# Optimization experiments

Hardware: AMD Instinct MI355X
Metric: run time of the kernel (lower is better)

Reference implementation:

```python
import jax, jax.numpy as jnp
import numpy as np

# --- config constants (from init_kwargs) ---
ALPHA = 0.05; SIGMA = 0.2; THETA = 0.3; A = 0.02; B_PAR = 0.1; RHO = 0.5
MULT = 2.0          # config.x_range_final[1]
GAMMA = 0.5         # power-utility exponent: u(x,r)=r*x^g/g, ux=r*x^(g-1)
N_STEPS = 100; T_FINAL = 1.0; DT = T_FINAL / N_STEPS
HID = 64; BATCH = 16384
PEN_SCALE = 100.0; LOWER = 1e-6


def _mlp(W1, b1, W2, b2, W3, b3, s):
    # tiny FeedForwardSubNet: 3 -> HID -> HID -> 1, tanh activations
    h = jnp.tanh(s @ W1 + b1)
    h = jnp.tanh(h @ W2 + b2)
    return h @ W3 + b3


def _penalise(v):
    # penalise_range(v, lower): quadratic hinge below `lower`
    return PEN_SCALE * jnp.square(jnp.maximum(LOWER - v, 0.0))


def setup_inputs() -> dict:
    key = jax.random.key(0)
    ks = jax.random.split(key, 16)
    dw = jax.random.normal(ks[0], (BATCH, 1, N_STEPS), dtype=jnp.float32) * float(np.sqrt(DT))
    X0 = jnp.ones((1,), jnp.float32)
    R0 = jnp.ones((1,), jnp.float32)
    def w(k, shape, fan):
        return jax.random.normal(k, shape, jnp.float32) / np.float32(np.sqrt(fan))
    inp = {"dw": dw, "X0": X0, "R0": R0,
           "pW1": w(ks[1], (3, HID), 3), "pb1": jnp.zeros((HID,), jnp.float32),
           "pW2": w(ks[2], (HID, HID), HID), "pb2": jnp.zeros((HID,), jnp.float32),
           "pW3": w(ks[3], (HID, 1), HID), "pb3": jnp.zeros((1,), jnp.float32),
           "qW1": w(ks[4], (3, HID), 3), "qb1": jnp.zeros((HID,), jnp.float32),
           "qW2": w(ks[5], (HID, HID), HID), "qb2": jnp.zeros((HID,), jnp.float32),
           "qW3": w(ks[6], (HID, 1), HID), "qb3": jnp.zeros((1,), jnp.float32)}
    return inp


def reference(dw, X0, R0, pW1, pb1, pW2, pb2, pW3, pb3, qW1, qb1, qW2, qb2, qW3, qb3):
    Bn = dw.shape[0]
    ones = jnp.ones((Bn, 1), dw.dtype)
    times = jnp.arange(N_STEPS + 1, dtype=dw.dtype) * DT   # [N+1]
    x0 = ones * X0
    R0v = ones * R0
    b_eff = float(np.sign(RHO)) * B_PAR

    # p_0 and dp_0 = d p_0 / d x (per-sample, rowwise independent net)
    def p_of_x(xx):
        st = jnp.concatenate([MULT * times[0] * ones, xx, R0v], 1)
        return _mlp(pW1, pb1, pW2, pb2, pW3, pb3, st)
    p0, p_vjp = jax.vjp(p_of_x, x0)
    (dp0,) = p_vjp(jnp.ones_like(p0))
    pi0 = _mlp(qW1, qb1, qW2, qb2, qW3, qb3,
               jnp.concatenate([MULT * times[0] * ones, x0, R0v], 1))

    dw_t = jnp.transpose(dw, (2, 0, 1))          # [N, B, 1]
    upd = jnp.arange(N_STEPS) < (N_STEPS - 1)    # pi not updated at last step

    def step(carry, inp):
        x, min_x, W, pi = carry
        dwi, t_next, u = inp
        x = x + x * ALPHA * DT + pi * SIGMA * THETA * DT + pi * SIGMA * dwi
        min_x = jnp.minimum(x, min_x)
        W = W + dwi
        Rv = R0v * jnp.exp((A - 0.5 * b_eff ** 2) * t_next + b_eff * W)
        p = p0 * jnp.exp(-(ALPHA + 0.5 * THETA ** 2) * t_next - THETA * W)
        st = jnp.concatenate([MULT * t_next * jnp.ones_like(x), x, Rv], 1)
        pi_new = _mlp(qW1, qb1, qW2, qb2, qW3, qb3, st)
        pi = jnp.where(u, pi_new, pi)
        return (x, min_x, W, pi), (x, Rv, pi, -p)

    (xf, min_x, Wf, pif), (xs, Rs, pis, dMs) = jax.lax.scan(
        step, (x0, x0, jnp.zeros_like(x0), pi0), (dw_t, times[1:], upd))

    # stacked process data, matching tf.concat-over-axis-0 ordering: [(N+1)*B, 1]
    x_all  = jnp.concatenate([x0[None], xs], 0).reshape(-1, 1)
    r_all  = jnp.concatenate([R0v[None], Rs], 0).reshape(-1, 1)
    pi_all = jnp.concatenate([pi0[None], pis], 0).reshape(-1, 1)
    dM_all = jnp.concatenate([(-p0)[None], dMs], 0).reshape(-1, 1)
    dM2_all = jnp.tile(-dp0, (N_STEPS + 1, 1))
    proc = jnp.concatenate([x_all, r_all, pi_all, dM_all, dM2_all], 1)  # [(N+1)*B, 5]

    # losses (non_concave = False branch)
    p_fin = -dMs[-1]
    R_fin = Rs[-1]
    xc = jnp.maximum(xf, LOWER)
    ux = R_fin * xc ** (GAMMA - 1.0)
    u_val = R_fin * xc ** GAMMA / GAMMA
    pen = _penalise(min_x)
    loss_p = jnp.mean(jnp.square(p_fin + ux) + pen)
    loss_pi = loss_p + jnp.mean(-u_val + pen)

    return jnp.concatenate([proc.reshape(-1), jnp.stack([loss_p, loss_pi])])
```

## Files before the change

kernel.cpp:

```cpp
#include <hip/hip_runtime.h>
#include <hip/hip_bf16.h>
#include <math.h>

#define NSTEP 100
#define BATCH 16384
#define MB 16
#define NBLK (BATCH/MB)
#define NT 256

#define C_ALPHA 0.05f
#define C_SIGMA 0.2f
#define C_THETA 0.3f
#define C_DT    0.01f
#define C_LOWER 1e-6f
#define C_PEN   100.0f
#define LOG2E   1.4426950408889634f
#define TSCALE  (2.0f * LOG2E)
#define CRT ( 0.015f * C_DT * LOG2E)
#define CRW ( 0.1f * LOG2E)
#define CPT (-0.095f * C_DT * LOG2E)
#define CPW (-0.3f * LOG2E)

#define TSC   64.0f
#define TOFF  512.0f
#define TMAX  1023.999f
#define AXD   (1.0f + C_ALPHA * C_DT)
#define SIGTHDT (C_SIGMA * C_THETA * C_DT)

#define WG_BARRIER() asm volatile("s_waitcnt lgkmcnt(0)\n\ts_barrier" ::: "memory")

typedef __attribute__((ext_vector_type(8))) short bf16x8;
typedef __attribute__((ext_vector_type(4))) float f32x4;
typedef __attribute__((ext_vector_type(4), aligned(4))) float f32x4a;

__device__ __forceinline__ float tanh_pre(float zs) {
    float e = __builtin_amdgcn_exp2f(zs);
    return 1.0f - 2.0f * __builtin_amdgcn_rcpf(e + 1.0f);
}
__device__ __forceinline__ unsigned f2bf_u(float f) {
    unsigned u = __float_as_uint(f);
    return (u + 0x7FFFu + ((u >> 16) & 1u)) >> 16;
}
__device__ __forceinline__ unsigned pack_bf16(float a, float b) {
    union { __hip_bfloat162 h; unsigned u; } cv;
    cv.h = __float22bfloat162_rn(make_float2(a, b));
    return cv.u;
}
__device__ __forceinline__ float dpp_row_sum16(float v) {
    int t;
    t = __builtin_amdgcn_update_dpp(0, __float_as_int(v), 0x128, 0xF, 0xF, true);
    v += __int_as_float(t);
    t = __builtin_amdgcn_update_dpp(0, __float_as_int(v), 0x124, 0xF, 0xF, true);
    v += __int_as_float(t);
    t = __builtin_amdgcn_update_dpp(0, __float_as_int(v), 0x122, 0xF, 0xF, true);
    v += __int_as_float(t);
    t = __builtin_amdgcn_update_dpp(0, __float_as_int(v), 0x121, 0xF, 0xF, true);
    v += __int_as_float(t);
    return v;
}

__global__ __launch_bounds__(NT, 4) void fused_kernel(
        const float* __restrict__ dw, const float* __restrict__ X0,
        const float* __restrict__ R0,
        const float* __restrict__ pW1, const float* __restrict__ pb1,
        const float* __restrict__ pW2, const float* __restrict__ pb2,
        const float* __restrict__ pW3, const float* __restrict__ pb3,
        const float* __restrict__ qW1, const float* __restrict__ qb1,
        const float* __restrict__ qW2, const float* __restrict__ qb2,
        const float* __restrict__ qW3, const float* __restrict__ qb3,
        float* __restrict__ ws, float* __restrict__ out) {
    __shared__ __align__(16) unsigned short sW2T[64 * 72];
    __shared__ __align__(16) float sdw[MB * NSTEP];
    __shared__ __align__(16) float2 sTab[1024];
    __shared__ __align__(16) uint2 sA2[2][2][64][2];
    __shared__ __align__(16) float sPb[2][2][16][2];

    const int tid = threadIdx.x;
    const int lane = tid & 63;
    const int wv = tid >> 6;
    const int ks_own = wv >> 1;
    const int half = wv & 1;
    const int b0 = blockIdx.x * MB;
    const int l15 = lane & 15, quad = lane >> 4;

    {
        const float4* g = (const float4*)(dw + (size_t)b0 * NSTEP);
        float4* s = (float4*)sdw;
        for (int u = tid; u < MB * NSTEP / 4; u += NT) s[u] = g[u];
    }
    for (int u4 = tid; u4 < 1024; u4 += NT) {
        float4 w = ((const float4*)qW2)[u4];
        int base = u4 * 4;
        int k = base >> 6, n = base & 63;
        sW2T[(n + 0) * 72 + k] = (unsigned short)f2bf_u(w.x * TSC);
        sW2T[(n + 1) * 72 + k] = (unsigned short)f2bf_u(w.y * TSC);
        sW2T[(n + 2) * 72 + k] = (unsigned short)f2bf_u(w.z * TSC);
        sW2T[(n + 3) * 72 + k] = (unsigned short)f2bf_u(w.w * TSC);
    }
    for (int u = tid; u < 1024; u += NT) {
        float z0 = (float)u * (1.0f / TSC) - 8.0f;
        float t0 = tanh_pre(TSCALE * z0);
        float t1 = tanh_pre(TSCALE * (z0 + 1.0f / TSC));
        sTab[u] = make_float2(t0, t1 - t0);
    }
    __syncthreads();

    auto tab = [&](float u) -> float {
        float uc = __builtin_amdgcn_fmed3f(u, 0.0f, TMAX);
        int idx = (int)uc;
        float f = uc - (float)idx;
        float2 e = sTab[idx];
        return fmaf(f, e.y, e.x);
    };

    bf16x8 Bw0, Bw1;
    {
        const unsigned short* rp = &sW2T[(wv * 16 + l15) * 72 + quad * 8];
        Bw0 = *(const bf16x8*)rp;
        Bw1 = *(const bf16x8*)(rp + 32);
    }
    float tco[4], w1xs[4], w1rs[4], b1s[4];
    {
        const int kb = ks_own * 32 + quad * 8 + half * 4;
        #pragma unroll
        for (int j = 0; j < 4; j++) {
            tco[j]  = qW1[kb + j] * (2.0f * C_DT * TSC);
            w1xs[j] = qW1[64 + kb + j] * TSC;
            w1rs[j] = qW1[128 + kb + j] * TSC;
            b1s[j]  = qb1[kb + j] * TSC + TOFF;
        }
    }
    f32x4 b2w;
    float w3w[4];
    #pragma unroll
    for (int r = 0; r < 4; r++) {
        b2w[r] = qb2[wv * 16 + quad * 4 + r] * TSC + TOFF;
        w3w[r] = qW3[wv * 16 + quad * 4 + r];
    }
    const float b3 = qb3[0];
    const float X0v = X0[0], R0s = R0[0];

    uint2*       wA0 = &sA2[0][ks_own][lane][half];
    uint2*       wA1 = &sA2[1][ks_own][lane][half];
    const uint2* rA0 = &sA2[0][0][lane][0];
    const uint2* rA1 = &sA2[1][0][lane][0];
    float*        wP0 = &sPb[0][wv >> 1][l15][wv & 1];
    float*        wP1 = &sPb[1][wv >> 1][l15][wv & 1];
    const float2* rP0 = (const float2*)&sPb[0][0][l15][0];
    const float2* rP1 = (const float2*)&sPb[1][0][l15][0];

    float p0, dp0;
    {
        float pre = fmaf(pW1[64 + lane], X0v, fmaf(pW1[128 + lane], R0s, pb1[lane]));
        float h1 = tanh_pre(TSCALE * pre);
        float d1 = (1.0f - h1 * h1) * pW1[64 + lane];
        float a0 = pb2[lane], a1 = 0.f, a2 = 0.f, a3 = 0.f;
        float e0 = 0.f, e1 = 0.f, e2 = 0.f, e3 = 0.f;
        for (int i2 = 0; i2 < 64; i2 += 4) {
            float w0 = pW2[(i2 + 0) * 64 + lane];
            float w1 = pW2[(i2 + 1) * 64 + lane];
            float w2 = pW2[(i2 + 2) * 64 + lane];
            float w3 = pW2[(i2 + 3) * 64 + lane];
            a0 = fmaf(__shfl(h1, i2 + 0), w0, a0); e0 = fmaf(__shfl(d1, i2 + 0), w0, e0);
            a1 = fmaf(__shfl(h1, i2 + 1), w1, a1); e1 = fmaf(__shfl(d1, i2 + 1), w1, e1);
            a2 = fmaf(__shfl(h1, i2 + 2), w2, a2); e2 = fmaf(__shfl(d1, i2 + 2), w2, e2);
            a3 = fmaf(__shfl(h1, i2 + 3), w3, a3); e3 = fmaf(__shfl(d1, i2 + 3), w3, e3);
        }
        float pre2 = (a0 + a1) + (a2 + a3);
        float dpre2 = (e0 + e1) + (e2 + e3);
        float h2 = tanh_pre(TSCALE * pre2);
        float d2 = (1.0f - h2 * h2) * dpre2;
        float c1 = h2 * pW3[lane], c2 = d2 * pW3[lane];
        #pragma unroll
        for (int o = 1; o < 64; o <<= 1) {
            c1 += __shfl_xor(c1, o);
            c2 += __shfl_xor(c2, o);
        }
        p0 = c1 + pb3[0]; dp0 = c2;
    }
    const float mdp0 = -dp0;

    auto qnet = [&](float fi, float xv, float rv, uint2* wA, const uint2* rA,
                    float* wP, const float2* rP) -> float {
        union { uint2 u2; unsigned u[2]; } Aloc;
        {
            float z0 = fmaf(w1xs[0], xv, fmaf(w1rs[0], rv, fmaf(tco[0], fi, b1s[0])));
            float z1 = fmaf(w1xs[1], xv, fmaf(w1rs[1], rv, fmaf(tco[1], fi, b1s[1])));
            float z2 = fmaf(w1xs[2], xv, fmaf(w1rs[2], rv, fmaf(tco[2], fi, b1s[2])));
            float z3 = fmaf(w1xs[3], xv, fmaf(w1rs[3], rv, fmaf(tco[3], fi, b1s[3])));
            Aloc.u[0] = pack_bf16(tab(z0), tab(z1));
            Aloc.u[1] = pack_bf16(tab(z2), tab(z3));
        }
        *wA = Aloc.u2;
        WG_BARRIER();
        bf16x8 A0 = *(const bf16x8*)rA;
        bf16x8 A1 = *(const bf16x8*)(rA + 128);
        f32x4 acc = b2w;
        acc = __builtin_amdgcn_mfma_f32_16x16x32_bf16(Bw0, A0, acc, 0, 0, 0);
        acc = __builtin_amdgcn_mfma_f32_16x16x32_bf16(Bw1, A1, acc, 0, 0, 0);
        float ps = fmaf(tab(acc[0]), w3w[0],
                   fmaf(tab(acc[1]), w3w[1],
                   fmaf(tab(acc[2]), w3w[2], tab(acc[3]) * w3w[3])));
        ps += __shfl_xor(ps, 16);
        ps += __shfl_xor(ps, 32);
        if (quad == 0) *wP = ps;
        WG_BARRIER();
        float2 pa = rP[0], pb = rP[16];
        return ((pa.x + pa.y) + (pb.x + pb.y)) + b3;
    };

    float x = X0v, minx = X0v;
    float pi = qnet(0.0f, X0v, R0s, wA0, rA0, wP0, rP0);
    float* op = out + (size_t)(b0 + l15) * 5;
    if (wv == 3) {
        if (quad == 0) {
            f32x4a o = {X0v, R0s, pi, -p0};
            *(f32x4a*)op = o;
        } else if (quad == 1) {
            op[4] = mdp0;
        }
    }

    const float* sdwp = &sdw[l15 * NSTEP];
    float dwc = sdwp[0];
    float Rn  = R0s * __builtin_amdgcn_exp2f(fmaf(CRW, dwc, CRT));
    float pmn = p0  * __builtin_amdgcn_exp2f(fmaf(CPW, dwc, CPT));
    float spn = fmaf(dwc, C_SIGMA, SIGTHDT);
    sdwp += 1;
    float fc = 1.0f;

    auto STEP = [&](uint2* wA, const uint2* rA, float* wP, const float2* rP) {
        float R = Rn, pm = pmn, sp = spn;
        float d2 = *sdwp++;
        Rn  *= __builtin_amdgcn_exp2f(fmaf(CRW, d2, CRT));
        pmn *= __builtin_amdgcn_exp2f(fmaf(CPW, d2, CPT));
        spn  = fmaf(d2, C_SIGMA, SIGTHDT);
        x = fmaf(x, AXD, pi * sp);
        minx = fminf(minx, x);
        float pin = qnet(fc, x, R, wA, rA, wP, rP);
        if (wv == 3) {
            op += (size_t)BATCH * 5;
            if (quad == 0) {
                f32x4a o = {x, R, pin, -pm};
                *(f32x4a*)op = o;
            } else if (quad == 1) {
                op[4] = mdp0;
            }
        }
        pi = pin;
        fc += 1.0f;
    };

    #pragma unroll 1
    for (int it = 0; it < 49; ++it) {
        STEP(wA1, rA1, wP1, rP1);
        STEP(wA0, rA0, wP0, rP0);
    }
    STEP(wA1, rA1, wP1, rP1);

    {
        x = fmaf(x, AXD, pi * spn);
        minx = fminf(minx, x);
        float Rf = Rn, pf = pmn;
        if (wv == 3) {
            op += (size_t)BATCH * 5;
            if (quad == 0) {
                f32x4a o = {x, Rf, pi, -pf};
                *(f32x4a*)op = o;
            } else if (quad == 1) {
                op[4] = mdp0;
            }
        }
        if (wv == 0) {
            float xc = fmaxf(x, C_LOWER);
            float ux = Rf * rsqrtf(xc);
            float uval = 2.0f * Rf * sqrtf(xc);
            float d = fmaxf(C_LOWER - minx, 0.0f);
            float pen = C_PEN * d * d;
            float t1 = pf + ux;
            float v1 = dpp_row_sum16(t1 * t1 + pen);
            float v2 = dpp_row_sum16(-uval + pen);
            if (lane == 0) {
                atomicAdd(&ws[3], v1);
                atomicAdd(&ws[4], v2);
                __threadfence();
                int old = atomicAdd((int*)(ws + 5), 1);
                if (old == NBLK - 1) {
                    float lp = atomicAdd(&ws[3], 0.0f) * (1.0f / (float)BATCH);
                    float lq = atomicAdd(&ws[4], 0.0f) * (1.0f / (float)BATCH);
                    out[(size_t)(NSTEP + 1) * BATCH * 5] = lp;
                    out[(size_t)(NSTEP + 1) * BATCH * 5 + 1] = lp + lq;
                }
            }
        }
    }
}

extern "C" void kernel_launch(void* const* d_in, const int* in_sizes, int n_in,
                              void* d_out, int out_size, void* d_ws, size_t ws_size,
                              hipStream_t stream) {
    const float* dw  = (const float*)d_in[0];
    const float* X0  = (const float*)d_in[1];
    const float* R0  = (const float*)d_in[2];
    const float* pW1 = (const float*)d_in[3];
    const float* pb1 = (const float*)d_in[4];
    const float* pW2 = (const float*)d_in[5];
    const float* pb2 = (const float*)d_in[6];
    const float* pW3 = (const float*)d_in[7];
    const float* pb3 = (const float*)d_in[8];
    const float* qW1 = (const float*)d_in[9];
    const float* qb1 = (const float*)d_in[10];
    const float* qW2 = (const float*)d_in[11];
    const float* qb2 = (const float*)d_in[12];
    const float* qW3 = (const float*)d_in[13];
    const float* qb3 = (const float*)d_in[14];
    float* out = (float*)d_out;
    float* ws  = (float*)d_ws;

    hipMemsetAsync(d_ws, 0, 64, stream);
    fused_kernel<<<NBLK, NT, 0, stream>>>(dw, X0, R0, pW1, pb1, pW2, pb2, pW3, pb3,
                                          qW1, qb1, qW2, qb2, qW3, qb3, ws, out);
}
```

Baseline: 198.7 us.

## Compute full second layer redundantly per wave to drop reduction barrier

Each wave now holds all four 16-column tiles of the second-layer weights and runs all eight MFMAs itself, finishing the output reduction with shuffles instead of a shared-memory partial-sum exchange. This removes one workgroup barrier and the LDS round trip in each of the 100 sequential steps. In exchange each wave does four times the MFMA and table-lookup work and holds more registers, so launch bounds drop to 3 waves per SIMD.

```diff
diff --git a/kernel.cpp b/kernel.cpp
--- a/kernel.cpp
+++ b/kernel.cpp
@@ -59,7 +59,7 @@
     return v;
 }
 
-__global__ __launch_bounds__(NT, 4) void fused_kernel(
+__global__ __launch_bounds__(NT, 3) void fused_kernel(
         const float* __restrict__ dw, const float* __restrict__ X0,
         const float* __restrict__ R0,
         const float* __restrict__ pW1, const float* __restrict__ pb1,
@@ -73,7 +73,6 @@
     __shared__ __align__(16) float sdw[MB * NSTEP];
     __shared__ __align__(16) float2 sTab[1024];
     __shared__ __align__(16) uint2 sA2[2][2][64][2];
-    __shared__ __align__(16) float sPb[2][2][16][2];
 
     const int tid = threadIdx.x;
     const int lane = tid & 63;
@@ -113,11 +112,12 @@
         return fmaf(f, e.y, e.x);
     };
 
-    bf16x8 Bw0, Bw1;
-    {
-        const unsigned short* rp = &sW2T[(wv * 16 + l15) * 72 + quad * 8];
-        Bw0 = *(const bf16x8*)rp;
-        Bw1 = *(const bf16x8*)(rp + 32);
+    bf16x8 Bw[4][2];
+    #pragma unroll
+    for (int nt = 0; nt < 4; nt++) {
+        const unsigned short* rp = &sW2T[(nt * 16 + l15) * 72 + quad * 8];
+        Bw[nt][0] = *(const bf16x8*)rp;
+        Bw[nt][1] = *(const bf16x8*)(rp + 32);
     }
     float tco[4], w1xs[4], w1rs[4], b1s[4];
     {
@@ -130,12 +130,15 @@
             b1s[j]  = qb1[kb + j] * TSC + TOFF;
         }
     }
-    f32x4 b2w;
-    float w3w[4];
+    f32x4 b2a[4];
+    float w3c[4][4];
     #pragma unroll
-    for (int r = 0; r < 4; r++) {
-        b2w[r] = qb2[wv * 16 + quad * 4 + r] * TSC + TOFF;
-        w3w[r] = qW3[wv * 16 + quad * 4 + r];
+    for (int nt = 0; nt < 4; nt++) {
+        #pragma unroll
+        for (int r = 0; r < 4; r++) {
+            b2a[nt][r] = qb2[nt * 16 + quad * 4 + r] * TSC + TOFF;
+            w3c[nt][r] = qW3[nt * 16 + quad * 4 + r];
+        }
     }
     const float b3 = qb3[0];
     const float X0v = X0[0], R0s = R0[0];
@@ -144,10 +147,6 @@
     uint2*       wA1 = &sA2[1][ks_own][lane][half];
     const uint2* rA0 = &sA2[0][0][lane][0];
     const uint2* rA1 = &sA2[1][0][lane][0];
-    float*        wP0 = &sPb[0][wv >> 1][l15][wv & 1];
-    float*        wP1 = &sPb[1][wv >> 1][l15][wv & 1];
-    const float2* rP0 = (const float2*)&sPb[0][0][l15][0];
-    const float2* rP1 = (const float2*)&sPb[1][0][l15][0];
 
     float p0, dp0;
     {
@@ -180,8 +179,7 @@
     }
     const float mdp0 = -dp0;
 
-    auto qnet = [&](float fi, float xv, float rv, uint2* wA, const uint2* rA,
-                    float* wP, const float2* rP) -> float {
+    auto qnet = [&](float fi, float xv, float rv, uint2* wA, const uint2* rA) -> float {
         union { uint2 u2; unsigned u[2]; } Aloc;
         {
             float z0 = fmaf(w1xs[0], xv, fmaf(w1rs[0], rv, fmaf(tco[0], fi, b1s[0])));
@@ -195,22 +193,25 @@
         WG_BARRIER();
         bf16x8 A0 = *(const bf16x8*)rA;
         bf16x8 A1 = *(const bf16x8*)(rA + 128);
-        f32x4 acc = b2w;
-        acc = __builtin_amdgcn_mfma_f32_16x16x32_bf16(Bw0, A0, acc, 0, 0, 0);
-        acc = __builtin_amdgcn_mfma_f32_16x16x32_bf16(Bw1, A1, acc, 0, 0, 0);
-        float ps = fmaf(tab(acc[0]), w3w[0],
-                   fmaf(tab(acc[1]), w3w[1],
-                   fmaf(tab(acc[2]), w3w[2], tab(acc[3]) * w3w[3])));
+        float ps0 = 0.f, ps1 = 0.f, ps2 = 0.f, ps3 = 0.f;
+        #pragma unroll
+        for (int nt = 0; nt < 4; nt++) {
+            f32x4 a = b2a[nt];
+            a = __builtin_amdgcn_mfma_f32_16x16x32_bf16(Bw[nt][0], A0, a, 0, 0, 0);
+            a = __builtin_amdgcn_mfma_f32_16x16x32_bf16(Bw[nt][1], A1, a, 0, 0, 0);
+            ps0 = fmaf(tab(a[0]), w3c[nt][0], ps0);
+            ps1 = fmaf(tab(a[1]), w3c[nt][1], ps1);
+            ps2 = fmaf(tab(a[2]), w3c[nt][2], ps2);
+            ps3 = fmaf(tab(a[3]), w3c[nt][3], ps3);
+        }
+        float ps = (ps0 + ps1) + (ps2 + ps3);
         ps += __shfl_xor(ps, 16);
         ps += __shfl_xor(ps, 32);
-        if (quad == 0) *wP = ps;
-        WG_BARRIER();
-        float2 pa = rP[0], pb = rP[16];
-        return ((pa.x + pa.y) + (pb.x + pb.y)) + b3;
+        return ps + b3;
     };
 
     float x = X0v, minx = X0v;
-    float pi = qnet(0.0f, X0v, R0s, wA0, rA0, wP0, rP0);
+    float pi = qnet(0.0f, X0v, R0s, wA0, rA0);
     float* op = out + (size_t)(b0 + l15) * 5;
     if (wv == 3) {
         if (quad == 0) {
@@ -229,7 +230,7 @@
     sdwp += 1;
     float fc = 1.0f;
 
-    auto STEP = [&](uint2* wA, const uint2* rA, float* wP, const float2* rP) {
+    auto STEP = [&](uint2* wA, const uint2* rA) {
         float R = Rn, pm = pmn, sp = spn;
         float d2 = *sdwp++;
         Rn  *= __builtin_amdgcn_exp2f(fmaf(CRW, d2, CRT));
@@ -237,7 +238,7 @@
         spn  = fmaf(d2, C_SIGMA, SIGTHDT);
         x = fmaf(x, AXD, pi * sp);
         minx = fminf(minx, x);
-        float pin = qnet(fc, x, R, wA, rA, wP, rP);
+        float pin = qnet(fc, x, R, wA, rA);
         if (wv == 3) {
             op += (size_t)BATCH * 5;
             if (quad == 0) {
@@ -253,10 +254,10 @@
 
     #pragma unroll 1
     for (int it = 0; it < 49; ++it) {
-        STEP(wA1, rA1, wP1, rP1);
-        STEP(wA0, rA0, wP0, rP0);
-    }
-    STEP(wA1, rA1, wP1, rP1);
+        STEP(wA1, rA1);
+        STEP(wA0, rA0);
+    }
+    STEP(wA1, rA1);
 
     {
         x = fmaf(x, AXD, pi * spn);
```

Result: slower. 248.4 us (+25.0%).
